# Performance work log

Hardware: AMD Instinct MI355X
Metric: run time of the kernel (lower is better)

Reference implementation:

```python
import jax, jax.numpy as jnp
import numpy as np

N_RAYS = 16384
T = 4194304          # total ragged samples across all rays (avg 256/ray)
M_PAD = 512          # static pad width, >= max per-ray count
STEPSIZE = 3.0 * np.sqrt(3.0) / 1024.0  # (aabb extent)*sqrt(3)/render_n_samples


def setup_inputs() -> dict:
    key = jax.random.key(0)
    k1, k2, k3 = jax.random.split(key, 3)
    rays = jax.random.normal(k1, (N_RAYS, 6), dtype=jnp.float32)
    dirs = rays[:, 3:6]
    dirs = dirs / jnp.linalg.norm(dirs, axis=-1, keepdims=True)
    rays_chunk = jnp.concatenate([rays[:, 0:3], dirs], axis=-1)
    # ragged sample list from ray_marching: sorted ray ids -> ragged counts
    ray_indices = jnp.sort(jax.random.randint(k2, (T,), 0, N_RAYS, dtype=jnp.int32))
    t_starts = jax.random.uniform(k3, (T,), jnp.float32, 0.1, 5.0)
    t_ends = t_starts + jnp.float32(STEPSIZE)
    return {"rays_chunk": rays_chunk, "ray_indices": ray_indices,
            "t_starts": t_starts, "t_ends": t_ends, "max_samps": M_PAD}


def reference(rays_chunk, ray_indices, t_starts, t_ends, max_samps):
    N = rays_chunk.shape[0]
    Tn = ray_indices.shape[0]
    origins = rays_chunk[:, 0:3]
    viewdirs = rays_chunk[:, 3:6]

    pz_vals = (t_starts + t_ends) * 0.5              # [T]
    pdists = t_ends - t_starts                       # [T]
    xyz = origins[ray_indices] + pz_vals[:, None] * viewdirs[ray_indices]  # [T,3]
    # append 0 size channel -> (M, 4) premasked valid sample points
    xyz_sampled = jnp.concatenate([xyz, jnp.zeros((Tn, 1), xyz.dtype)], axis=-1)

    # per-ray counts (== torch.unique(..., return_counts=True) scattered to N)
    counts = jax.ops.segment_sum(jnp.ones((Tn,), jnp.int32), ray_indices,
                                 num_segments=N)                 # [N]
    offsets = jnp.cumsum(counts) - counts                        # exclusive cumsum
    pos = jnp.arange(Tn, dtype=jnp.int32) - offsets[ray_indices] # slot within ray

    ray_valid = jnp.arange(max_samps)[None, :] < counts[:, None] # [N, M] bool

    # boolean-mask scatters dists[ray_valid]=pdists etc., done as indexed scatter
    z_vals = jnp.zeros((N, max_samps), t_starts.dtype).at[ray_indices, pos].set(pz_vals)
    dists = jnp.zeros((N, max_samps), t_starts.dtype).at[ray_indices, pos].set(pdists)
    xyz_sampled_w = jnp.zeros((N, max_samps, 4), xyz.dtype).at[ray_indices, pos].set(xyz_sampled)

    whole_valid = jnp.ones((N,), dtype=bool)
    # original returns (xyzs, ray_valid, M, z_vals, dists, whole_valid);
    # M is the static pad width here; xyz_sampled_w appended to keep the
    # padded-scatter path (the kernel-headroom op) live.
    return (xyz_sampled, ray_valid, z_vals, dists, whole_valid, xyz_sampled_w)
```

## Files before the change

### kernel.cpp

```cpp
#include <hip/hip_runtime.h>

#define M_PAD 512

typedef float f32x4 __attribute__((ext_vector_type(4)));

__device__ __forceinline__ int lower_bound_wave(const int* __restrict__ ri,
                                                int Tn, int target, int lane) {
    int lo = 0, hi = Tn;
    while (hi - lo > 64) {
        int len = hi - lo;
        int probe = lo + (len * (lane + 1)) / 65;
        int v = ri[probe];
        unsigned long long m = __ballot(v < target);
        int k = __popcll(m);
        int nlo = (k == 0)  ? lo : lo + (len * k) / 65;
        int nhi = (k == 64) ? hi : lo + (len * (k + 1)) / 65;
        lo = nlo; hi = nhi;
    }
    int p = lo + lane;
    int v = (p < hi) ? ri[p] : 2147483647;
    unsigned long long m = __ballot(v < target);
    return lo + __popcll(m);
}

__global__ __launch_bounds__(256)
void mono_kernel(const float* __restrict__ rays,
                 const int* __restrict__ ri,
                 const float* __restrict__ ts,
                 const float* __restrict__ te,
                 float* __restrict__ xyz_out,
                 float* __restrict__ ray_valid,
                 float* __restrict__ z_vals,
                 float* __restrict__ dists,
                 float* __restrict__ xyz_w,
                 float* __restrict__ whole_valid,
                 int T) {
    const int b = blockIdx.x;
    const int r = b >> 1;
    const int h = b & 1;
    const int tid = threadIdx.x;
    const int wave = tid >> 6, lane = tid & 63;

    __shared__ int sh[2];
    if (wave < 2) {
        int lb = lower_bound_wave(ri, T, r + wave, lane);
        if (lane == 0) sh[wave] = lb;
    }
    __syncthreads();
    const int s = sh[0];
    const int cnt = sh[1] - s;

    const int j = h * 256 + tid;
    const int idx = (r << 9) + j;

    float z = 0.0f, dd = 0.0f, v = 0.0f;
    f32x4 pt = {0.f, 0.f, 0.f, 0.f};

    if (j < cnt) {
        int i = s + j;
        float a = ts[i], bb = te[i];
        z  = (a + bb) * 0.5f;
        dd = bb - a;
        v  = 1.0f;
        const float* rc = rays + (size_t)r * 6;
        pt.x = fmaf(z, rc[3], rc[0]);
        pt.y = fmaf(z, rc[4], rc[1]);
        pt.z = fmaf(z, rc[5], rc[2]);
        __builtin_nontemporal_store(pt, reinterpret_cast<f32x4*>(xyz_out) + i);
    }

    __builtin_nontemporal_store(z,  &z_vals[idx]);
    __builtin_nontemporal_store(dd, &dists[idx]);
    __builtin_nontemporal_store(v,  &ray_valid[idx]);
    __builtin_nontemporal_store(pt, reinterpret_cast<f32x4*>(xyz_w) + idx);

    if (j == 0) whole_valid[r] = 1.0f;
}

extern "C" void kernel_launch(void* const* d_in, const int* in_sizes, int n_in,
                              void* d_out, int out_size, void* d_ws, size_t ws_size,
                              hipStream_t stream) {
    const float* rays = (const float*)d_in[0];
    const int*   ri   = (const int*)d_in[1];
    const float* ts   = (const float*)d_in[2];
    const float* te   = (const float*)d_in[3];
    const int N = in_sizes[0] / 6;
    const int T = in_sizes[1];

    float* out         = (float*)d_out;
    float* xyz_out     = out;
    float* ray_valid   = xyz_out + (size_t)T * 4;
    float* z_vals      = ray_valid + (size_t)N * M_PAD;
    float* dists       = z_vals + (size_t)N * M_PAD;
    float* whole_valid = dists + (size_t)N * M_PAD;
    float* xyz_w       = whole_valid + N;

    mono_kernel<<<N * 2, 256, 0, stream>>>(rays, ri, ts, te,
                                           xyz_out, ray_valid, z_vals,
                                           dists, xyz_w, whole_valid, T);
}
```

Before: 69.03 us.

## Seed ray-segment binary search from uniform guess and process two rays per block

Each block now handles two full rays with 1024 threads, so three boundaries are searched per block instead of two per half-ray block, which cuts redundant searches roughly fourfold. The lower-bound search starts from a guess proportional to target*T/N and widens a window until it brackets the answer, which shortens the search range and the dependent global loads. The guess assumes roughly uniform ray ids; skewed distributions fall back to widening rounds. The launch also assumes N is even.

```diff
diff --git a/kernel.cpp b/kernel.cpp
--- a/kernel.cpp
+++ b/kernel.cpp
@@ -4,9 +4,19 @@
 
 typedef float f32x4 __attribute__((ext_vector_type(4)));
 
-__device__ __forceinline__ int lower_bound_wave(const int* __restrict__ ri,
-                                                int Tn, int target, int lane) {
-    int lo = 0, hi = Tn;
+__device__ __forceinline__ int lower_bound_seeded(const int* __restrict__ ri,
+                                                  int T, int N, int target,
+                                                  int lane) {
+    int guess = (int)(((long long)target * T) / N);
+    int W = 4096;
+    int lo = max(0, guess - W), hi = min(T, guess + W);
+    while (true) {
+        bool okLo = (lo == 0) || (ri[lo - 1] < target);
+        bool okHi = (hi == T) || (ri[hi] >= target);
+        if (okLo && okHi) break;
+        W <<= 3;
+        lo = max(0, guess - W); hi = min(T, guess + W);
+    }
     while (hi - lo > 64) {
         int len = hi - lo;
         int probe = lo + (len * (lane + 1)) / 65;
@@ -23,7 +33,7 @@
     return lo + __popcll(m);
 }
 
-__global__ __launch_bounds__(256)
+__global__ __launch_bounds__(1024)
 void mono_kernel(const float* __restrict__ rays,
                  const int* __restrict__ ri,
                  const float* __restrict__ ts,
@@ -34,23 +44,23 @@
                  float* __restrict__ dists,
                  float* __restrict__ xyz_w,
                  float* __restrict__ whole_valid,
-                 int T) {
-    const int b = blockIdx.x;
-    const int r = b >> 1;
-    const int h = b & 1;
+                 int N, int T) {
+    const int r0 = blockIdx.x * 2;
     const int tid = threadIdx.x;
     const int wave = tid >> 6, lane = tid & 63;
 
-    __shared__ int sh[2];
-    if (wave < 2) {
-        int lb = lower_bound_wave(ri, T, r + wave, lane);
+    __shared__ int sh[3];
+    if (wave < 3) {
+        int lb = lower_bound_seeded(ri, T, N, r0 + wave, lane);
         if (lane == 0) sh[wave] = lb;
     }
     __syncthreads();
-    const int s = sh[0];
-    const int cnt = sh[1] - s;
 
-    const int j = h * 256 + tid;
+    const int k = tid >> 9;
+    const int j = tid & (M_PAD - 1);
+    const int r = r0 + k;
+    const int s = sh[k];
+    const int cnt = sh[k + 1] - s;
     const int idx = (r << 9) + j;
 
     float z = 0.0f, dd = 0.0f, v = 0.0f;
@@ -95,7 +105,7 @@
     float* whole_valid = dists + (size_t)N * M_PAD;
     float* xyz_w       = whole_valid + N;
 
-    mono_kernel<<<N * 2, 256, 0, stream>>>(rays, ri, ts, te,
-                                           xyz_out, ray_valid, z_vals,
-                                           dists, xyz_w, whole_valid, T);
+    mono_kernel<<<N / 2, 1024, 0, stream>>>(rays, ri, ts, te,
+                                            xyz_out, ray_valid, z_vals,
+                                            dists, xyz_w, whole_valid, N, T);
 }
```

Result: no change. 69.20 us (+0.2%).
